# Kernel optimization log

Hardware: AMD Instinct MI355X
Metric: run time of the kernel (lower is better)

Reference implementation:

```python
import jax, jax.numpy as jnp
import numpy as np

N_OBJ, N_REG = 4096, 8192
D_HO = D_HR = 512
GATE_W = 128
E = 131072


def setup_inputs() -> dict:
    key = jax.random.key(0)
    ks = jax.random.split(key, 10)
    s = 1.0 / np.sqrt(D_HO + D_HR)
    return {
        "feature_obj": jax.random.normal(ks[0], (N_OBJ, D_HO), jnp.float32),
        "feature_region": jax.random.normal(ks[1], (N_REG, D_HR), jnp.float32),
        # edge lists (tgt, src) equivalent to np.where(select_mat > 0)
        "r2o_tgt": jnp.sort(jax.random.randint(ks[2], (E,), 0, N_OBJ, jnp.int32)),
        "r2o_src": jax.random.randint(ks[3], (E,), 0, N_REG, jnp.int32),
        "o2r_tgt": jnp.sort(jax.random.randint(ks[4], (E,), 0, N_REG, jnp.int32)),
        "o2r_src": jax.random.randint(ks[5], (E,), 0, N_OBJ, jnp.int32),
        # attention gate Linear(dim_src+dim_tgt -> gate_width), bias=True
        "gw_r2o": jax.random.uniform(ks[6], (GATE_W, D_HR + D_HO), jnp.float32, -s, s),
        "gb_r2o": jnp.zeros((GATE_W,), jnp.float32),
        "gw_o2r": jax.random.uniform(ks[7], (GATE_W, D_HO + D_HR), jnp.float32, -s, s),
        "gb_o2r": jnp.zeros((GATE_W,), jnp.float32),
        # transform Sequential(ReLU, Linear(dim -> dim, bias=True))
        "tw_r2o": jax.random.uniform(ks[8], (D_HO, D_HR), jnp.float32, -s, s),
        "tb_r2o": jnp.zeros((D_HO,), jnp.float32),
        "tw_o2r": jax.random.uniform(ks[9], (D_HR, D_HO), jnp.float32, -s, s),
        "tb_o2r": jnp.zeros((D_HR,), jnp.float32),
    }


def _message(tgt_feat, src_feat, tgt_idx, src_idx, gw, gb, num_tgt):
    # gather per-edge source/target features: [E, ds], [E, dt]
    src = src_feat[src_idx]
    tgt = tgt_feat[tgt_idx]
    # Attention_Module: gate = mean(sigmoid(W @ relu(cat(src, tgt)) + b))
    g = jax.nn.relu(jnp.concatenate([src, tgt], axis=-1))
    gate = jnp.mean(jax.nn.sigmoid(g @ gw.T + gb), axis=-1, keepdims=True)  # [E, 1]
    msg = src * gate
    agg = jax.ops.segment_sum(msg, tgt_idx, num_segments=num_tgt)
    # mps_use_average=True -> per-target mean; targets with no edges stay zero
    cnt = jax.ops.segment_sum(jnp.ones((tgt_idx.shape[0], 1), msg.dtype), tgt_idx, num_segments=num_tgt)
    return agg / jnp.maximum(cnt, 1.0)


def reference(feature_obj, feature_region, r2o_tgt, r2o_src, o2r_tgt, o2r_src,
              gw_r2o, gb_r2o, gw_o2r, gb_o2r, tw_r2o, tb_r2o, tw_o2r, tb_o2r):
    m_r2o = _message(feature_obj, feature_region, r2o_tgt, r2o_src, gw_r2o, gb_r2o, N_OBJ)
    out_obj = feature_obj + jax.nn.relu(m_r2o) @ tw_r2o.T + tb_r2o
    m_o2r = _message(feature_region, feature_obj, o2r_tgt, o2r_src, gw_o2r, gb_o2r, N_REG)
    out_reg = feature_region + jax.nn.relu(m_o2r) @ tw_o2r.T + tb_o2r
    return (out_obj, out_reg)
```

## Files before the change

### kernel.cpp

```cpp
#include <hip/hip_runtime.h>

constexpr int N_OBJ = 4096, N_REG = 8192, D = 512, GW = 128, NE = 131072;

typedef __attribute__((ext_vector_type(8))) short short8;
typedef __attribute__((ext_vector_type(4))) float f32x4;
typedef __attribute__((ext_vector_type(2))) float f32x2;

__device__ inline short f2bf(float f) {
  unsigned u = __builtin_bit_cast(unsigned, f);
  unsigned r = (u + 0x7FFF + ((u >> 16) & 1)) >> 16;
  return (short)r;
}
__device__ inline float bf2f(short s) {
  return __builtin_bit_cast(float, (unsigned)(((unsigned short)s) << 16));
}

__global__ __launch_bounds__(256) void cast_csr(
    const float* __restrict__ feat_reg, const float* __restrict__ feat_obj,
    const float* __restrict__ gw_r2o, const float* __restrict__ gw_o2r,
    const float* __restrict__ tw_r2o, const float* __restrict__ tw_o2r,
    const int* __restrict__ t_r2o, const int* __restrict__ t_o2r,
    unsigned char* __restrict__ raw_reg, short* __restrict__ relu_reg,
    unsigned char* __restrict__ raw_obj, short* __restrict__ relu_obj,
    short* __restrict__ Wreg, short* __restrict__ Wobj,
    short* __restrict__ btw_r2o, short* __restrict__ btw_o2r,
    int* __restrict__ off_r2o, int* __restrict__ off_o2r) {
  int i = blockIdx.x * 256 + threadIdx.x;
  if (i >= 1769472) {
    i -= 1769472;
    const int* tgt; int* off; int t;
    if (i <= N_OBJ) { tgt = t_r2o; off = off_r2o; t = i; }
    else {
      i -= N_OBJ + 1;
      if (i > N_REG) return;
      tgt = t_o2r; off = off_o2r; t = i;
    }
    int lo = 0, hi = NE;
    while (lo < hi) {
      int mid = (lo + hi) >> 1;
      if (tgt[mid] < t) lo = mid + 1; else hi = mid;
    }
    off[t] = lo;
    return;
  }
  if (i < 1572864) {
    const float* src; unsigned char* draw; short* drelu; int j = i;
    if (j < 1048576) { src = feat_reg; draw = raw_reg; drelu = relu_reg; }
    else { j -= 1048576; src = feat_obj; draw = raw_obj; drelu = relu_obj; }
    float4 v = ((const float4*)src)[j];
    int p = __builtin_amdgcn_cvt_pk_fp8_f32(v.x, v.y, 0, false);
    p = __builtin_amdgcn_cvt_pk_fp8_f32(v.z, v.w, p, true);
    ((unsigned*)draw)[j] = (unsigned)p;
    ((short4*)drelu)[j] = make_short4(f2bf(fmaxf(v.x, 0.f)), f2bf(fmaxf(v.y, 0.f)),
                                      f2bf(fmaxf(v.z, 0.f)), f2bf(fmaxf(v.w, 0.f)));
    return;
  }
  i -= 1572864;
  const float* src; short* dst; int di;
  if (i < 32768) {
    int row = i >> 7, c4 = i & 127;
    src = (row < 128) ? gw_r2o + (size_t)row * 1024 + c4 * 4
                      : gw_o2r + (size_t)(row - 128) * 1024 + 512 + c4 * 4;
    dst = Wreg; di = i;
  } else if (i < 65536) {
    int k = i - 32768, row = k >> 7, c4 = k & 127;
    src = (row < 128) ? gw_r2o + (size_t)row * 1024 + 512 + c4 * 4
                      : gw_o2r + (size_t)(row - 128) * 1024 + c4 * 4;
    dst = Wobj; di = k;
  } else if (i < 131072) { di = i - 65536; src = tw_r2o + (size_t)di * 4; dst = btw_r2o; }
  else                   { di = i - 131072; src = tw_o2r + (size_t)di * 4; dst = btw_o2r; }
  float4 v = *(const float4*)src;
  ((short4*)dst)[di] = make_short4(f2bf(v.x), f2bf(v.y), f2bf(v.z), f2bf(v.w));
}

struct GemmPair {
  const short* A[2]; const short* B[2];
  const float* res[2]; const float* bias[2];
  void* C[2];
  int nb0;
  int nxb;
  int ldc;
};

template<bool EPI>
__global__ __launch_bounds__(256) void gemm_pair(GemmPair gp) {
  __shared__ short As[128 * 32];
  __shared__ short Bs[128 * 32];
  int b = blockIdx.x;
  const int pi = (b >= gp.nb0) ? 1 : 0;
  if (pi) b -= gp.nb0;
  const int bx = b % gp.nxb, by = b / gp.nxb;
  const short* __restrict__ A = gp.A[pi];
  const short* __restrict__ B = gp.B[pi];
  const int ldc = gp.ldc;
  const int tid = threadIdx.x;
  const int lane = tid & 63, w = tid >> 6;
  const int m0 = by * 128, n0 = bx * 128;
  const int wm = (w >> 1) * 64, wn = (w & 1) * 64;
  const int sr = lane >> 2, sc = (lane & 3) * 8;
  const int fr = lane & 15, fk = (lane >> 4) * 8;

  f32x4 acc[4][4];
#pragma unroll
  for (int i = 0; i < 4; ++i)
#pragma unroll
    for (int j = 0; j < 4; ++j) acc[i][j] = (f32x4){0.f, 0.f, 0.f, 0.f};

  for (int k0 = 0; k0 < 512; k0 += 32) {
#pragma unroll
    for (int h = 0; h < 2; ++h) {
      int rg = w * 32 + h * 16;
      const short* ga = A + (size_t)(m0 + rg + sr) * 512 + k0 + sc;
      const short* gb = B + (size_t)(n0 + rg + sr) * 512 + k0 + sc;
      __builtin_amdgcn_global_load_lds(
          (const __attribute__((address_space(1))) void*)ga,
          (__attribute__((address_space(3))) void*)&As[rg * 32], 16, 0, 0);
      __builtin_amdgcn_global_load_lds(
          (const __attribute__((address_space(1))) void*)gb,
          (__attribute__((address_space(3))) void*)&Bs[rg * 32], 16, 0, 0);
    }
    __syncthreads();
    short8 a[4], bfr[4];
#pragma unroll
    for (int i = 0; i < 4; ++i)
      a[i] = *(const short8*)&As[(wm + i * 16 + fr) * 32 + fk];
#pragma unroll
    for (int j = 0; j < 4; ++j)
      bfr[j] = *(const short8*)&Bs[(wn + j * 16 + fr) * 32 + fk];
#pragma unroll
    for (int i = 0; i < 4; ++i)
#pragma unroll
      for (int j = 0; j < 4; ++j)
        acc[i][j] = __builtin_amdgcn_mfma_f32_16x16x32_bf16(a[i], bfr[j], acc[i][j], 0, 0, 0);
    __syncthreads();
  }

  if (EPI) {
    float* C = (float*)gp.C[pi];
    const float* res = gp.res[pi];
    const float* bias = gp.bias[pi];
#pragma unroll
    for (int i = 0; i < 4; ++i)
#pragma unroll
      for (int j = 0; j < 4; ++j) {
        int n = n0 + wn + j * 16 + fr;
#pragma unroll
        for (int r = 0; r < 4; ++r) {
          int m = m0 + wm + i * 16 + (lane >> 4) * 4 + r;
          C[(size_t)m * ldc + n] = acc[i][j][r] + res[(size_t)m * ldc + n] + bias[n];
        }
      }
  } else {
    unsigned char* C = (unsigned char*)gp.C[pi];
#pragma unroll
    for (int i = 0; i < 4; ++i)
#pragma unroll
      for (int j = 0; j < 4; ++j) {
        int n = n0 + wn + j * 16 + fr;
#pragma unroll
        for (int r = 0; r < 4; ++r) {
          int m = m0 + wm + i * 16 + (lane >> 4) * 4 + r;
          int pk = __builtin_amdgcn_cvt_pk_fp8_f32(acc[i][j][r], acc[i][j][r], 0, false);
          C[(size_t)m * ldc + n] = (unsigned char)(pk & 0xFF);
        }
      }
  }
}

__global__ __launch_bounds__(256) void fused_msg(
    const unsigned char* __restrict__ Preg, const unsigned char* __restrict__ Pobj,
    const unsigned char* __restrict__ raw_reg, const unsigned char* __restrict__ raw_obj,
    const int* __restrict__ r2o_src, const int* __restrict__ o2r_src,
    const int* __restrict__ off_r2o, const int* __restrict__ off_o2r,
    const float* __restrict__ gb_r2o, const float* __restrict__ gb_o2r,
    short* __restrict__ m_obj, short* __restrict__ m_reg) {
  __shared__ float red[4][512];
  int t = blockIdx.x;
  const unsigned char *PA, *PB, *feat; const int *src, *off; const float* gb;
  short* mo; int po;
  if (t < N_OBJ) {
    PA = Preg; PB = Pobj; feat = raw_reg; src = r2o_src; off = off_r2o;
    gb = gb_r2o; mo = m_obj; po = 0;
  } else {
    t -= N_OBJ;
    PA = Pobj; PB = Preg; feat = raw_obj; src = o2r_src; off = off_o2r;
    gb = gb_o2r; mo = m_reg; po = 128;
  }
  const int tid = threadIdx.x, lane = tid & 63, w = tid >> 6;
  const int hw = lane >> 5, l = lane & 31;
  const int e0 = off[t], e1 = off[t + 1];
  unsigned pbu = *(const unsigned*)&PB[(size_t)t * 256 + po + l * 4];
  f32x2 pb01 = __builtin_amdgcn_cvt_pk_f32_fp8((int)pbu, false);
  f32x2 pb23 = __builtin_amdgcn_cvt_pk_f32_fp8((int)pbu, true);
  float4 gbv = *(const float4*)&gb[l * 4];
  const float c0 = pb01.x + gbv.x, c1 = pb01.y + gbv.y;
  const float c2 = pb23.x + gbv.z, c3 = pb23.y + gbv.w;
  float acc[16] = {};
  for (int e = e0 + w * 2 + hw; e < e1; e += 8) {
    int s = src[e];
    unsigned pau = *(const unsigned*)&PA[(size_t)s * 256 + po + l * 4];
    uint4 fv = *(const uint4*)&feat[(size_t)s * 512 + l * 16];
    f32x2 a01 = __builtin_amdgcn_cvt_pk_f32_fp8((int)pau, false);
    f32x2 a23 = __builtin_amdgcn_cvt_pk_f32_fp8((int)pau, true);
    float gs = 1.f / (1.f + __expf(-(a01.x + c0)))
             + 1.f / (1.f + __expf(-(a01.y + c1)))
             + 1.f / (1.f + __expf(-(a23.x + c2)))
             + 1.f / (1.f + __expf(-(a23.y + c3)));
#pragma unroll
    for (int msk = 16; msk >= 1; msk >>= 1) gs += __shfl_xor(gs, msk, 64);
    f32x2 f0 = __builtin_amdgcn_cvt_pk_f32_fp8((int)fv.x, false);
    f32x2 f1 = __builtin_amdgcn_cvt_pk_f32_fp8((int)fv.x, true);
    f32x2 f2 = __builtin_amdgcn_cvt_pk_f32_fp8((int)fv.y, false);
    f32x2 f3 = __builtin_amdgcn_cvt_pk_f32_fp8((int)fv.y, true);
    f32x2 f4 = __builtin_amdgcn_cvt_pk_f32_fp8((int)fv.z, false);
    f32x2 f5 = __builtin_amdgcn_cvt_pk_f32_fp8((int)fv.z, true);
    f32x2 f6 = __builtin_amdgcn_cvt_pk_f32_fp8((int)fv.w, false);
    f32x2 f7 = __builtin_amdgcn_cvt_pk_f32_fp8((int)fv.w, true);
    acc[0]  += f0.x * gs; acc[1]  += f0.y * gs;
    acc[2]  += f1.x * gs; acc[3]  += f1.y * gs;
    acc[4]  += f2.x * gs; acc[5]  += f2.y * gs;
    acc[6]  += f3.x * gs; acc[7]  += f3.y * gs;
    acc[8]  += f4.x * gs; acc[9]  += f4.y * gs;
    acc[10] += f5.x * gs; acc[11] += f5.y * gs;
    acc[12] += f6.x * gs; acc[13] += f6.y * gs;
    acc[14] += f7.x * gs; acc[15] += f7.y * gs;
  }
#pragma unroll
  for (int jj = 0; jj < 16; ++jj) acc[jj] += __shfl_xor(acc[jj], 32, 64);
  if (hw == 0) {
#pragma unroll
    for (int q = 0; q < 4; ++q)
      *(float4*)&red[w][l * 16 + q * 4] =
          (float4){acc[q * 4], acc[q * 4 + 1], acc[q * 4 + 2], acc[q * 4 + 3]};
  }
  __syncthreads();
  const float inv = (1.0f / 128.0f) / fmaxf((float)(e1 - e0), 1.0f);
  const int d = tid * 2;
  float s0 = red[0][d] + red[1][d] + red[2][d] + red[3][d];
  float s1 = red[0][d + 1] + red[1][d + 1] + red[2][d + 1] + red[3][d + 1];
  short2 o;
  o.x = f2bf(fmaxf(s0 * inv, 0.f));
  o.y = f2bf(fmaxf(s1 * inv, 0.f));
  *(short2*)(mo + (size_t)t * 512 + d) = o;
}

extern "C" void kernel_launch(void* const* d_in, const int* in_sizes, int n_in,
                              void* d_out, int out_size, void* d_ws, size_t ws_size,
                              hipStream_t stream) {
  const float* feat_obj = (const float*)d_in[0];
  const float* feat_reg = (const float*)d_in[1];
  const int*   r2o_tgt  = (const int*)d_in[2];
  const int*   r2o_src  = (const int*)d_in[3];
  const int*   o2r_tgt  = (const int*)d_in[4];
  const int*   o2r_src  = (const int*)d_in[5];
  const float* gw_r2o   = (const float*)d_in[6];
  const float* gb_r2o   = (const float*)d_in[7];
  const float* gw_o2r   = (const float*)d_in[8];
  const float* gb_o2r   = (const float*)d_in[9];
  const float* tw_r2o   = (const float*)d_in[10];
  const float* tb_r2o   = (const float*)d_in[11];
  const float* tw_o2r   = (const float*)d_in[12];
  const float* tb_o2r   = (const float*)d_in[13];
  float* out_obj = (float*)d_out;
  float* out_reg = out_obj + (size_t)N_OBJ * D;

  size_t cur = 0;
  auto alloc = [&](size_t bytes) -> void* {
    cur = (cur + 255) & ~(size_t)255;
    void* p = (char*)d_ws + cur;
    cur += bytes;
    return p;
  };
  int*   off_r2o = (int*)alloc((N_OBJ + 1) * sizeof(int));
  int*   off_o2r = (int*)alloc((N_REG + 1) * sizeof(int));
  unsigned char* raw_reg = (unsigned char*)alloc((size_t)N_REG * D);
  unsigned char* raw_obj = (unsigned char*)alloc((size_t)N_OBJ * D);
  short* relu_reg= (short*)alloc((size_t)N_REG * D * 2);
  short* relu_obj= (short*)alloc((size_t)N_OBJ * D * 2);
  short* Wreg    = (short*)alloc((size_t)256 * D * 2);
  short* Wobj    = (short*)alloc((size_t)256 * D * 2);
  short* btw_r2o = (short*)alloc((size_t)D * D * 2);
  short* btw_o2r = (short*)alloc((size_t)D * D * 2);
  unsigned char* Preg = (unsigned char*)alloc((size_t)N_REG * 256);
  unsigned char* Pobj = (unsigned char*)alloc((size_t)N_OBJ * 256);
  short* m_obj   = (short*)alloc((size_t)N_OBJ * D * 2);
  short* m_reg   = (short*)alloc((size_t)N_REG * D * 2);

  cast_csr<<<6961, 256, 0, stream>>>(feat_reg, feat_obj, gw_r2o, gw_o2r, tw_r2o, tw_o2r,
                                     r2o_tgt, o2r_tgt,
                                     raw_reg, relu_reg, raw_obj, relu_obj,
                                     Wreg, Wobj, btw_r2o, btw_o2r, off_r2o, off_o2r);

  GemmPair proj;
  proj.A[0] = relu_reg; proj.B[0] = Wreg; proj.C[0] = Preg;
  proj.A[1] = relu_obj; proj.B[1] = Wobj; proj.C[1] = Pobj;
  proj.res[0] = proj.res[1] = nullptr; proj.bias[0] = proj.bias[1] = nullptr;
  proj.nb0 = 2 * (N_REG / 128); proj.nxb = 2; proj.ldc = 256;
  gemm_pair<false><<<192, 256, 0, stream>>>(proj);

  fused_msg<<<N_OBJ + N_REG, 256, 0, stream>>>(Preg, Pobj, raw_reg, raw_obj,
                                               r2o_src, o2r_src, off_r2o, off_o2r,
                                               gb_r2o, gb_o2r, m_obj, m_reg);

  GemmPair tr;
  tr.A[0] = m_reg; tr.B[0] = btw_o2r; tr.res[0] = feat_reg; tr.bias[0] = tb_o2r; tr.C[0] = out_reg;
  tr.A[1] = m_obj; tr.B[1] = btw_r2o; tr.res[1] = feat_obj; tr.bias[1] = tb_r2o; tr.C[1] = out_obj;
  tr.nb0 = 4 * (N_REG / 128); tr.nxb = 4; tr.ldc = D;
  gemm_pair<true><<<384, 256, 0, stream>>>(tr);
}
```

Before: 186.0 us.

## Double-buffer GEMM LDS tiles, narrow projection tiles, and unroll edge loop

The GEMM kernel now double-buffers its LDS tiles, so the next k-slice loads while the current one feeds MFMA, and it takes a template BN. The projection GEMM uses 128x64 tiles, doubling its grid to 384 blocks for better CU occupancy. The message kernel processes two edges per iteration to overlap gathers and the shuffle reductions, and it uses a hardware reciprocal in the sigmoid. These changes cost more LDS and registers per block, and the reciprocal is slightly less accurate.

```diff
diff --git a/kernel.cpp b/kernel.cpp
--- a/kernel.cpp
+++ b/kernel.cpp
@@ -10,9 +10,6 @@
   unsigned u = __builtin_bit_cast(unsigned, f);
   unsigned r = (u + 0x7FFF + ((u >> 16) & 1)) >> 16;
   return (short)r;
-}
-__device__ inline float bf2f(short s) {
-  return __builtin_bit_cast(float, (unsigned)(((unsigned short)s) << 16));
 }
 
 __global__ __launch_bounds__(256) void cast_csr(
@@ -82,10 +79,11 @@
   int ldc;
 };
 
-template<bool EPI>
+template<bool EPI, int BN>
 __global__ __launch_bounds__(256) void gemm_pair(GemmPair gp) {
-  __shared__ short As[128 * 32];
-  __shared__ short Bs[128 * 32];
+  constexpr int NF = BN / 32;
+  __shared__ short As[2][128 * 32];
+  __shared__ short Bs[2][BN * 32];
   int b = blockIdx.x;
   const int pi = (b >= gp.nb0) ? 1 : 0;
   if (pi) b -= gp.nb0;
@@ -95,45 +93,60 @@
   const int ldc = gp.ldc;
   const int tid = threadIdx.x;
   const int lane = tid & 63, w = tid >> 6;
-  const int m0 = by * 128, n0 = bx * 128;
-  const int wm = (w >> 1) * 64, wn = (w & 1) * 64;
+  const int m0 = by * 128, n0 = bx * BN;
+  const int wm = (w >> 1) * 64, wn = (w & 1) * (BN / 2);
   const int sr = lane >> 2, sc = (lane & 3) * 8;
   const int fr = lane & 15, fk = (lane >> 4) * 8;
 
-  f32x4 acc[4][4];
+  f32x4 acc[4][NF];
 #pragma unroll
   for (int i = 0; i < 4; ++i)
 #pragma unroll
-    for (int j = 0; j < 4; ++j) acc[i][j] = (f32x4){0.f, 0.f, 0.f, 0.f};
-
-  for (int k0 = 0; k0 < 512; k0 += 32) {
+    for (int j = 0; j < NF; ++j) acc[i][j] = (f32x4){0.f, 0.f, 0.f, 0.f};
+
+  auto stage = [&](int buf, int k0) {
 #pragma unroll
     for (int h = 0; h < 2; ++h) {
       int rg = w * 32 + h * 16;
       const short* ga = A + (size_t)(m0 + rg + sr) * 512 + k0 + sc;
+      __builtin_amdgcn_global_load_lds(
+          (const __attribute__((address_space(1))) void*)ga,
+          (__attribute__((address_space(3))) void*)&As[buf][rg * 32], 16, 0, 0);
+    }
+#pragma unroll
+    for (int h = 0; h < BN / 64; ++h) {
+      int rg = w * (BN / 4) + h * 16;
       const short* gb = B + (size_t)(n0 + rg + sr) * 512 + k0 + sc;
       __builtin_amdgcn_global_load_lds(
-          (const __attribute__((address_space(1))) void*)ga,
-          (__attribute__((address_space(3))) void*)&As[rg * 32], 16, 0, 0);
-      __builtin_amdgcn_global_load_lds(
           (const __attribute__((address_space(1))) void*)gb,
-          (__attribute__((address_space(3))) void*)&Bs[rg * 32], 16, 0, 0);
-    }
+          (__attribute__((address_space(3))) void*)&Bs[buf][rg * 32], 16, 0, 0);
+    }
+  };
+  auto compute = [&](int buf) {
+    short8 a[4], bb[NF];
+#pragma unroll
+    for (int i = 0; i < 4; ++i)
+      a[i] = *(const short8*)&As[buf][(wm + i * 16 + fr) * 32 + fk];
+#pragma unroll
+    for (int j = 0; j < NF; ++j)
+      bb[j] = *(const short8*)&Bs[buf][(wn + j * 16 + fr) * 32 + fk];
+#pragma unroll
+    for (int i = 0; i < 4; ++i)
+#pragma unroll
+      for (int j = 0; j < NF; ++j)
+        acc[i][j] = __builtin_amdgcn_mfma_f32_16x16x32_bf16(a[i], bb[j], acc[i][j], 0, 0, 0);
+  };
+
+  stage(0, 0);
+  __syncthreads();
+  int cur = 0;
+  for (int k0 = 0; k0 < 512 - 32; k0 += 32) {
+    stage(cur ^ 1, k0 + 32);
+    compute(cur);
     __syncthreads();
-    short8 a[4], bfr[4];
-#pragma unroll
-    for (int i = 0; i < 4; ++i)
-      a[i] = *(const short8*)&As[(wm + i * 16 + fr) * 32 + fk];
-#pragma unroll
-    for (int j = 0; j < 4; ++j)
-      bfr[j] = *(const short8*)&Bs[(wn + j * 16 + fr) * 32 + fk];
-#pragma unroll
-    for (int i = 0; i < 4; ++i)
-#pragma unroll
-      for (int j = 0; j < 4; ++j)
-        acc[i][j] = __builtin_amdgcn_mfma_f32_16x16x32_bf16(a[i], bfr[j], acc[i][j], 0, 0, 0);
-    __syncthreads();
-  }
+    cur ^= 1;
+  }
+  compute(cur);
 
   if (EPI) {
     float* C = (float*)gp.C[pi];
@@ -142,7 +155,7 @@
 #pragma unroll
     for (int i = 0; i < 4; ++i)
 #pragma unroll
-      for (int j = 0; j < 4; ++j) {
+      for (int j = 0; j < NF; ++j) {
         int n = n0 + wn + j * 16 + fr;
 #pragma unroll
         for (int r = 0; r < 4; ++r) {
@@ -155,7 +168,7 @@
 #pragma unroll
     for (int i = 0; i < 4; ++i)
 #pragma unroll
-      for (int j = 0; j < 4; ++j) {
+      for (int j = 0; j < NF; ++j) {
         int n = n0 + wn + j * 16 + fr;
 #pragma unroll
         for (int r = 0; r < 4; ++r) {
@@ -196,18 +209,16 @@
   const float c0 = pb01.x + gbv.x, c1 = pb01.y + gbv.y;
   const float c2 = pb23.x + gbv.z, c3 = pb23.y + gbv.w;
   float acc[16] = {};
-  for (int e = e0 + w * 2 + hw; e < e1; e += 8) {
-    int s = src[e];
-    unsigned pau = *(const unsigned*)&PA[(size_t)s * 256 + po + l * 4];
-    uint4 fv = *(const uint4*)&feat[(size_t)s * 512 + l * 16];
+
+  auto sig4 = [&](unsigned pau) -> float {
     f32x2 a01 = __builtin_amdgcn_cvt_pk_f32_fp8((int)pau, false);
     f32x2 a23 = __builtin_amdgcn_cvt_pk_f32_fp8((int)pau, true);
-    float gs = 1.f / (1.f + __expf(-(a01.x + c0)))
-             + 1.f / (1.f + __expf(-(a01.y + c1)))
-             + 1.f / (1.f + __expf(-(a23.x + c2)))
-             + 1.f / (1.f + __expf(-(a23.y + c3)));
-#pragma unroll
-    for (int msk = 16; msk >= 1; msk >>= 1) gs += __shfl_xor(gs, msk, 64);
+    return __builtin_amdgcn_rcpf(1.f + __expf(-(a01.x + c0)))
+         + __builtin_amdgcn_rcpf(1.f + __expf(-(a01.y + c1)))
+         + __builtin_amdgcn_rcpf(1.f + __expf(-(a23.x + c2)))
+         + __builtin_amdgcn_rcpf(1.f + __expf(-(a23.y + c3)));
+  };
+  auto accum = [&](uint4 fv, float gs) {
     f32x2 f0 = __builtin_amdgcn_cvt_pk_f32_fp8((int)fv.x, false);
     f32x2 f1 = __builtin_amdgcn_cvt_pk_f32_fp8((int)fv.x, true);
     f32x2 f2 = __builtin_amdgcn_cvt_pk_f32_fp8((int)fv.y, false);
@@ -224,6 +235,32 @@
     acc[10] += f5.x * gs; acc[11] += f5.y * gs;
     acc[12] += f6.x * gs; acc[13] += f6.y * gs;
     acc[14] += f7.x * gs; acc[15] += f7.y * gs;
+  };
+
+  int e = e0 + w * 2 + hw;
+  for (; e + 8 < e1; e += 16) {
+    int s0 = src[e], s1 = src[e + 8];
+    unsigned pau0 = *(const unsigned*)&PA[(size_t)s0 * 256 + po + l * 4];
+    uint4 fv0 = *(const uint4*)&feat[(size_t)s0 * 512 + l * 16];
+    unsigned pau1 = *(const unsigned*)&PA[(size_t)s1 * 256 + po + l * 4];
+    uint4 fv1 = *(const uint4*)&feat[(size_t)s1 * 512 + l * 16];
+    float gs0 = sig4(pau0), gs1 = sig4(pau1);
+#pragma unroll
+    for (int msk = 16; msk >= 1; msk >>= 1) {
+      gs0 += __shfl_xor(gs0, msk, 64);
+      gs1 += __shfl_xor(gs1, msk, 64);
+    }
+    accum(fv0, gs0);
+    accum(fv1, gs1);
+  }
+  for (; e < e1; e += 8) {
+    int s = src[e];
+    unsigned pau = *(const unsigned*)&PA[(size_t)s * 256 + po + l * 4];
+    uint4 fv = *(const uint4*)&feat[(size_t)s * 512 + l * 16];
+    float gs = sig4(pau);
+#pragma unroll
+    for (int msk = 16; msk >= 1; msk >>= 1) gs += __shfl_xor(gs, msk, 64);
+    accum(fv, gs);
   }
 #pragma unroll
   for (int jj = 0; jj < 16; ++jj) acc[jj] += __shfl_xor(acc[jj], 32, 64);
@@ -295,8 +332,8 @@
   proj.A[0] = relu_reg; proj.B[0] = Wreg; proj.C[0] = Preg;
   proj.A[1] = relu_obj; proj.B[1] = Wobj; proj.C[1] = Pobj;
   proj.res[0] = proj.res[1] = nullptr; proj.bias[0] = proj.bias[1] = nullptr;
-  proj.nb0 = 2 * (N_REG / 128); proj.nxb = 2; proj.ldc = 256;
-  gemm_pair<false><<<192, 256, 0, stream>>>(proj);
+  proj.nb0 = 4 * (N_REG / 128); proj.nxb = 4; proj.ldc = 256;
+  gemm_pair<false, 64><<<384, 256, 0, stream>>>(proj);
 
   fused_msg<<<N_OBJ + N_REG, 256, 0, stream>>>(Preg, Pobj, raw_reg, raw_obj,
                                                r2o_src, o2r_src, off_r2o, off_o2r,
@@ -306,5 +343,5 @@
   tr.A[0] = m_reg; tr.B[0] = btw_o2r; tr.res[0] = feat_reg; tr.bias[0] = tb_o2r; tr.C[0] = out_reg;
   tr.A[1] = m_obj; tr.B[1] = btw_r2o; tr.res[1] = feat_obj; tr.bias[1] = tb_r2o; tr.C[1] = out_obj;
   tr.nb0 = 4 * (N_REG / 128); tr.nxb = 4; tr.ldc = D;
-  gemm_pair<true><<<384, 256, 0, stream>>>(tr);
-}
+  gemm_pair<true, 128><<<384, 256, 0, stream>>>(tr);
+}
```

Result: no change. 188.6 us, median of 2 (+1.4%).
